# Optimization experiments

Measured on AMD Instinct MI355X. Metric: run time of the kernel, lower is better.

The kernel has to match this reference:

```python
import jax, jax.numpy as jnp
import numpy as np

IMG_SIZE = 640.0
CONF_THRESH = 0.001
NMS_THRESH = 0.6
TOP_K = 1000  # fixed-shape candidate cap per class


def _pairwise_iou(b):
    # b: [K,4] in x1,y1,x2,y2; replicates the numpy NMS math (1e-28 / 1e-14 eps)
    x1, y1, x2, y2 = b[:, 0], b[:, 1], b[:, 2], b[:, 3]
    areas = (x2 - x1) * (y2 - y1)
    xx1 = jnp.maximum(x1[:, None], x1[None, :])
    yy1 = jnp.maximum(y1[:, None], y1[None, :])
    xx2 = jnp.minimum(x2[:, None], x2[None, :])
    yy2 = jnp.minimum(y2[:, None], y2[None, :])
    w = jnp.maximum(1e-28, xx2 - xx1)
    h = jnp.maximum(1e-28, yy2 - yy1)
    inter = w * h
    return inter / (areas[:, None] + areas[None, :] - inter + 1e-14)


def setup_inputs() -> dict:
    key = jax.random.key(0)
    k1, k2, k3 = jax.random.split(key, 3)
    img_size, strides, KA, C = 640, [8, 16, 32], 3, 80
    anchor = np.array([[10, 13], [16, 30], [33, 23], [30, 61], [62, 45], [59, 119],
                       [116, 90], [156, 198], [373, 326]], np.float32).reshape(3, 3, 2)
    grids, anchs, strs = [], [], []
    for lvl, s in enumerate(strides):
        f = img_size // s
        gy, gx = np.meshgrid(np.arange(f), np.arange(f), indexing='ij')
        gxy = np.stack([gx, gy], -1).reshape(-1, 1, 2).astype(np.float32)
        grids.append(np.broadcast_to(gxy, (f * f, KA, 2)).reshape(-1, 2))
        anchs.append(np.broadcast_to(anchor[lvl][None], (f * f, KA, 2)).reshape(-1, 2).astype(np.float32))
        strs.append(np.full((f * f * KA, 1), s, np.float32))
    grid_xy = jnp.asarray(np.concatenate(grids, 0))      # [N,2]
    anchors_wh = jnp.asarray(np.concatenate(anchs, 0))   # [N,2]
    stride_t = jnp.asarray(np.concatenate(strs, 0))      # [N,1]
    N = grid_xy.shape[0]  # 25200
    return {
        'reg_pred': jax.random.normal(k1, (N, 4), jnp.float32),
        'obj_pred': jax.random.normal(k2, (N, 1), jnp.float32),
        'cls_pred': jax.random.normal(k3, (N, C), jnp.float32),
        'grid_xy': grid_xy,
        'anchors_wh': anchors_wh,
        'stride_t': stride_t,
    }


def reference(reg_pred, obj_pred, cls_pred, grid_xy, anchors_wh, stride_t):
    # ---- box decode (YOLO head) ----
    xy = (jax.nn.sigmoid(reg_pred[:, :2]) + grid_xy) * stride_t       # centers in pixels
    wh = jnp.exp(reg_pred[:, 2:]) * anchors_wh                        # sizes in pixels
    boxes = jnp.concatenate([xy - 0.5 * wh, xy + 0.5 * wh], axis=-1)  # [N,4]
    boxes = jnp.clip(boxes / IMG_SIZE, 0.0, 1.0)
    # ---- scoring: sigmoid(obj) * softmax(cls) ----
    scores_all = jax.nn.sigmoid(obj_pred) * jax.nn.softmax(cls_pred, axis=-1)  # [N,C]
    cls_inds = jnp.argmax(scores_all, axis=-1)          # [N]
    scores = jnp.max(scores_all, axis=-1)               # [N]
    C = cls_pred.shape[-1]
    K = TOP_K
    ar = jnp.arange(K)

    def nms_class(c):
        s_c = jnp.where((cls_inds == c) & (scores >= CONF_THRESH), scores, -1.0)
        vals, idx = jax.lax.top_k(s_c, K)               # sorted desc, fixed shape
        b = boxes[idx]                                  # [K,4]
        valid = vals > 0.0
        iou = _pairwise_iou(b)                          # [K,K]

        def body(i, keep):
            sup = keep[i] & (iou[i] > NMS_THRESH) & (ar > i)
            return keep & ~sup

        keep = jax.lax.fori_loop(0, K, body, valid)
        return b, vals, keep

    boxes_out, scores_out, keep = jax.vmap(nms_class)(jnp.arange(C))  # [C,K,4],[C,K],[C,K]
    return boxes_out, scores_out * keep.astype(scores_out.dtype), keep
```

## Files before the change

### kernel.cpp

```cpp
#include <hip/hip_runtime.h>
#include <cstdint>
#include <cstddef>

#define N_CLS 80
#define TOPK 1000
#define POOL_N 2048
#define MCAP 512
#define BD 1024
#define DTB 128
#define NBLK 197
#define SLICE 32
#define LDSB_STRIDE 10

__global__ __launch_bounds__(DTB) void decode_kernel(
    const float* __restrict__ reg, const float* __restrict__ obj,
    const float* __restrict__ cls, const float* __restrict__ grid,
    const float* __restrict__ anch, const float* __restrict__ strd,
    float* __restrict__ boxes, uint2* __restrict__ scs,
    int* __restrict__ cnts, uint2* __restrict__ gpool2, int N) {
  __shared__ int hcnt[N_CLS];
  const int blk = blockIdx.x;
  const int tid = threadIdx.x;
  const int i = blk * DTB + tid;

  if (tid < N_CLS) hcnt[tid] = 0;
  __syncthreads();

  const bool valid = (i < N);
  float best = -1.0f;
  int bc = 0;

  if (valid) {
    const float4 r = ((const float4*)reg)[i];
    const float2 g = ((const float2*)grid)[i];
    const float2 aw = ((const float2*)anch)[i];
    const float st = strd[i];

    float cx = (1.0f / (1.0f + expf(-r.x)) + g.x) * st;
    float cy = (1.0f / (1.0f + expf(-r.y)) + g.y) * st;
    float w = expf(r.z) * aw.x;
    float h = expf(r.w) * aw.y;
    float b0 = fminf(fmaxf((cx - 0.5f * w) / 640.0f, 0.0f), 1.0f);
    float b1 = fminf(fmaxf((cy - 0.5f * h) / 640.0f, 0.0f), 1.0f);
    float b2 = fminf(fmaxf((cx + 0.5f * w) / 640.0f, 0.0f), 1.0f);
    float b3 = fminf(fmaxf((cy + 0.5f * h) / 640.0f, 0.0f), 1.0f);
    float4 bo; bo.x = b0; bo.y = b1; bo.z = b2; bo.w = b3;
    ((float4*)boxes)[i] = bo;

    const float4* cr = (const float4*)cls + (size_t)i * 20;
    float4 x[20];
#pragma unroll
    for (int q = 0; q < 20; ++q) x[q] = cr[q];

    float4 m4 = x[0];
#pragma unroll
    for (int q = 1; q < 20; ++q) {
      m4.x = fmaxf(m4.x, x[q].x); m4.y = fmaxf(m4.y, x[q].y);
      m4.z = fmaxf(m4.z, x[q].z); m4.w = fmaxf(m4.w, x[q].w);
    }
    float mx = fmaxf(fmaxf(m4.x, m4.y), fmaxf(m4.z, m4.w));

#pragma unroll
    for (int q = 0; q < 20; ++q) {
      x[q].x = expf(x[q].x - mx); x[q].y = expf(x[q].y - mx);
      x[q].z = expf(x[q].z - mx); x[q].w = expf(x[q].w - mx);
    }

    float s = 0.0f;
#pragma unroll
    for (int q = 0; q < 20; ++q) {
      s += x[q].x; s += x[q].y; s += x[q].z; s += x[q].w;
    }

    float sig = 1.0f / (1.0f + expf(-obj[i]));

#pragma unroll
    for (int q = 0; q < 20; ++q) {
      float q0 = sig * (x[q].x / s);
      if (q0 > best) { best = q0; bc = 4 * q + 0; }
      float q1 = sig * (x[q].y / s);
      if (q1 > best) { best = q1; bc = 4 * q + 1; }
      float q2 = sig * (x[q].z / s);
      if (q2 > best) { best = q2; bc = 4 * q + 2; }
      float q3 = sig * (x[q].w / s);
      if (q3 > best) { best = q3; bc = 4 * q + 3; }
    }
    scs[i] = make_uint2(__float_as_uint(best), (unsigned)bc);
  }

  const bool pos = valid && (best >= 0.001f);
  int slot = -1;
  if (pos) slot = atomicAdd(&hcnt[bc], 1);
  __syncthreads();
  if (tid < N_CLS) cnts[tid * NBLK + blk] = min(hcnt[tid], SLICE);
  if (pos && slot < SLICE)
    gpool2[((size_t)bc * NBLK + blk) * SLICE + slot] =
        make_uint2(__float_as_uint(best), (unsigned)i);
}

__device__ __forceinline__ unsigned long long kinit(int w, int m) {
  int lo = w << 6;
  return (m <= lo) ? 0ULL : ((m - lo >= 64) ? ~0ULL : ((1ULL << (m - lo)) - 1ULL));
}

__global__ __launch_bounds__(BD) void nms_kernel(
    const float* __restrict__ boxes, const uint2* __restrict__ scs,
    const int* __restrict__ cnts, const uint2* __restrict__ gpool2,
    float* __restrict__ out, int N) {
  const int c = blockIdx.x;
  const int tid = threadIdx.x;

  __shared__ uint2 pool[POOL_N];
  __shared__ float svals[TOPK];
  __shared__ int sidx[TOPK];
  __shared__ __align__(16) float4 bxyz[TOPK];
  __shared__ __align__(16) unsigned long long ldsB[MCAP * LDSB_STRIDE];
  __shared__ unsigned char kp[TOPK];
  __shared__ __align__(16) unsigned long long kmbuf[2][8];
  __shared__ int wsum[BD / 64 + 1];
  __shared__ int pref[NBLK + 1];

  if (tid < 64) {
    const int* cc = cnts + c * NBLK;
    int carry = 0;
    if (tid == 0) pref[0] = 0;
    for (int ch = 0; ch < (NBLK + 63) / 64; ++ch) {
      int b = ch * 64 + tid;
      int v = (b < NBLK) ? cc[b] : 0;
#pragma unroll
      for (int s = 1; s < 64; s <<= 1) {
        int u = __shfl_up(v, s, 64);
        if (tid >= (unsigned)s) v += u;
      }
      if (b < NBLK) pref[b + 1] = min(carry + v, POOL_N);
      carry += __shfl(v, 63, 64);
    }
  }
  __syncthreads();
  const int cnt = pref[NBLK];
  const int m = min(cnt, TOPK);

  const uint2* gp = gpool2 + (size_t)c * NBLK * SLICE;
  for (int t = tid; t < cnt; t += BD) {
    int lo = 0, hi = NBLK;
    while (hi - lo > 1) {
      int mid = (lo + hi) >> 1;
      if (t >= pref[mid]) lo = mid; else hi = mid;
    }
    pool[t] = gp[(size_t)lo * SLICE + (t - pref[lo])];
  }
  __syncthreads();

  for (int e = tid; e < cnt; e += BD) {
    uint2 me = pool[e];
    float v = __uint_as_float(me.x);
    int idx = (int)me.y;
    int r = 0;
#pragma unroll 8
    for (int k = 0; k < cnt; ++k) {
      uint2 q = pool[k];
      float vk = __uint_as_float(q.x);
      r += (int)((vk > v) || (vk == v && (int)q.y < idx));
    }
    if (r < TOPK) { svals[r] = v; sidx[r] = idx; }
  }
  __syncthreads();

  const int M = TOPK - m;
  if (M > 0) {
    int i = tid;
    bool f = false;
    if (i < N) {
      uint2 sc = scs[i];
      f = !((int)sc.y == c && __uint_as_float(sc.x) >= 0.001f);
    }
    unsigned long long mk = __ballot(f ? 1 : 0);
    int lane = tid & 63, wv = tid >> 6;
    int pre = __popcll(mk & ((1ULL << lane) - 1ULL));
    if (lane == 0) wsum[wv] = __popcll(mk);
    __syncthreads();
    if (tid == 0) {
      int acc = 0;
      for (int wq = 0; wq < BD / 64; ++wq) { int t2 = wsum[wq]; wsum[wq] = acc; acc += t2; }
    }
    __syncthreads();
    int pos = wsum[wv] + pre;
    if (f && pos < M) sidx[m + pos] = i;
  }
  __syncthreads();

  const float4* bf4 = (const float4*)boxes;
  for (int t = tid; t < TOPK; t += BD) bxyz[t] = bf4[sidx[t]];
  __syncthreads();

  const int W = (m + 63) >> 6;
  const bool fast = (m > 0) && (m <= MCAP);
  int cur = 0;

  if (fast) {
    const int tasks = m * W;
    for (int q = tid; q < tasks; q += BD) {
      int w = q / m;
      int j = q - w * m;
      unsigned long long bits = 0ULL;
      if (w <= (j >> 6)) {
        float4 jb = bxyz[j];
        float aj = (jb.z - jb.x) * (jb.w - jb.y);
        int i0 = w << 6, iend = min(i0 + 64, j);
        for (int i = i0; i < iend; ++i) {
          float4 ib = bxyz[i];
          float ai = (ib.z - ib.x) * (ib.w - ib.y);
          float xx1 = fmaxf(ib.x, jb.x), yy1 = fmaxf(ib.y, jb.y);
          float xx2 = fminf(ib.z, jb.z), yy2 = fminf(ib.w, jb.w);
          float ww = fmaxf(1e-28f, xx2 - xx1), hh = fmaxf(1e-28f, yy2 - yy1);
          float inter = ww * hh;
          float iou = inter / (ai + aj - inter + 1e-14f);
          if (iou > 0.6f) bits |= (1ULL << (i - i0));
        }
      }
      ldsB[(size_t)j * LDSB_STRIDE + w] = bits;
    }
    __syncthreads();

    ulonglong2 ta, tb, tc, td;
    ta = tb = tc = td = make_ulonglong2(0ULL, 0ULL);
    if (tid < m) {
      const ulonglong2* rp = (const ulonglong2*)&ldsB[(size_t)tid * LDSB_STRIDE];
      ta = rp[0]; tb = rp[1]; tc = rp[2]; td = rp[3];
    }
    if (tid < 8) kmbuf[0][tid] = kinit(tid, m);
    __syncthreads();

    for (;;) {
      bool keep = false;
      if (tid < m) {
        unsigned long long sup =
            (ta.x & kmbuf[cur][0]) | (ta.y & kmbuf[cur][1]) |
            (tb.x & kmbuf[cur][2]) | (tb.y & kmbuf[cur][3]) |
            (tc.x & kmbuf[cur][4]) | (tc.y & kmbuf[cur][5]) |
            (td.x & kmbuf[cur][6]) | (td.y & kmbuf[cur][7]);
        keep = (sup == 0ULL);
      }
      bool old = (tid < m) &&
                 ((kmbuf[cur][tid >> 6] >> (tid & 63)) & 1ULL);
      unsigned long long bl = __ballot(keep ? 1 : 0);
      int wv = tid >> 6;
      if ((tid & 63) == 0 && wv < 8) kmbuf[cur ^ 1][wv] = bl;
      int any = __syncthreads_or((int)(keep != old));
      cur ^= 1;
      if (!any) break;
    }
  } else {
    for (int t = tid; t < TOPK; t += BD) kp[t] = (t < m) ? 1 : 0;
    __syncthreads();
    for (int i = 0; i < m; ++i) {
      if (kp[i]) {
        float4 rb = bxyz[i];
        float ai = (rb.z - rb.x) * (rb.w - rb.y);
        for (int j = i + 1 + tid; j < m; j += BD) {
          if (kp[j]) {
            float4 jb = bxyz[j];
            float aj = (jb.z - jb.x) * (jb.w - jb.y);
            float xx1 = fmaxf(rb.x, jb.x), yy1 = fmaxf(rb.y, jb.y);
            float xx2 = fminf(rb.z, jb.z), yy2 = fminf(rb.w, jb.w);
            float ww = fmaxf(1e-28f, xx2 - xx1), hh = fmaxf(1e-28f, yy2 - yy1);
            float inter = ww * hh;
            float iou = inter / (ai + aj - inter + 1e-14f);
            if (iou > 0.6f) kp[j] = 0;
          }
        }
      }
      __syncthreads();
    }
  }

  float* outB = out;
  float* outS = out + N_CLS * TOPK * 4;
  float* outK = outS + N_CLS * TOPK;
  for (int t = tid; t < TOPK; t += BD) {
    float k = 0.0f;
    if (t < m)
      k = fast ? (float)((kmbuf[cur][t >> 6] >> (t & 63)) & 1ULL)
               : (float)kp[t];
    float v = (t < m) ? svals[t] : -1.0f;
    ((float4*)outB)[c * TOPK + t] = bxyz[t];
    outS[c * TOPK + t] = v * k;
    outK[c * TOPK + t] = k;
  }
}

extern "C" void kernel_launch(void* const* d_in, const int* in_sizes, int n_in,
                              void* d_out, int out_size, void* d_ws, size_t ws_size,
                              hipStream_t stream) {
  const float* reg  = (const float*)d_in[0];
  const float* obj  = (const float*)d_in[1];
  const float* cls  = (const float*)d_in[2];
  const float* grid = (const float*)d_in[3];
  const float* anch = (const float*)d_in[4];
  const float* strd = (const float*)d_in[5];
  const int N = in_sizes[0] / 4;

  char* w8 = (char*)d_ws;
  size_t off = 0;
  float* boxes  = (float*)(w8 + off); off += (size_t)N * 16;
  uint2* scs    = (uint2*)(w8 + off); off += (size_t)N * 8;
  int*   cnts   = (int*)(w8 + off);   off += (size_t)N_CLS * NBLK * 4;
  uint2* gpool2 = (uint2*)(w8 + off); off += (size_t)N_CLS * NBLK * SLICE * 8;
  float* out = (float*)d_out;

  decode_kernel<<<NBLK, DTB, 0, stream>>>(
      reg, obj, cls, grid, anch, strd, boxes, scs, cnts, gpool2, N);
  nms_kernel<<<N_CLS, BD, 0, stream>>>(boxes, scs, cnts, gpool2, out, N);
}
```

Before: 113.6 us.

## Fuse decode and NMS into one cooperative kernel with grid sync

Merges the decode and per-class NMS kernels into a single cooperative launch of 80 blocks, separated by a grid-wide barrier. This removes the second kernel launch and the gap between the two kernels. In exchange, decode runs on only 80 blocks with most threads idle. Each block now covers more elements but keeps the same 32-per-class slice cap, which can drop candidates that the earlier layout kept.

```diff
diff --git a/kernel.cpp b/kernel.cpp
--- a/kernel.cpp
+++ b/kernel.cpp
@@ -1,32 +1,52 @@
 #include <hip/hip_runtime.h>
+#include <hip/hip_cooperative_groups.h>
 #include <cstdint>
 #include <cstddef>
+
+namespace cg = cooperative_groups;
 
 #define N_CLS 80
 #define TOPK 1000
 #define POOL_N 2048
 #define MCAP 512
 #define BD 1024
-#define DTB 128
-#define NBLK 197
+#define NBLK 80
 #define SLICE 32
 #define LDSB_STRIDE 10
 
-__global__ __launch_bounds__(DTB) void decode_kernel(
+__device__ __forceinline__ unsigned long long kinit(int w, int m) {
+  int lo = w << 6;
+  return (m <= lo) ? 0ULL : ((m - lo >= 64) ? ~0ULL : ((1ULL << (m - lo)) - 1ULL));
+}
+
+__global__ __launch_bounds__(BD) void fused_kernel(
     const float* __restrict__ reg, const float* __restrict__ obj,
     const float* __restrict__ cls, const float* __restrict__ grid,
     const float* __restrict__ anch, const float* __restrict__ strd,
     float* __restrict__ boxes, uint2* __restrict__ scs,
-    int* __restrict__ cnts, uint2* __restrict__ gpool2, int N) {
-  __shared__ int hcnt[N_CLS];
+    int* __restrict__ cnts, uint2* __restrict__ gpool2,
+    float* __restrict__ out, int N) {
   const int blk = blockIdx.x;
   const int tid = threadIdx.x;
-  const int i = blk * DTB + tid;
+
+  __shared__ int hcnt[N_CLS];
+  __shared__ uint2 pool[POOL_N];
+  __shared__ float svals[TOPK];
+  __shared__ int sidx[TOPK];
+  __shared__ __align__(16) float4 bxyz[TOPK];
+  __shared__ __align__(16) unsigned long long ldsB[MCAP * LDSB_STRIDE];
+  __shared__ unsigned char kp[TOPK];
+  __shared__ __align__(16) unsigned long long kmbuf[2][8];
+  __shared__ int wsum[BD / 64 + 1];
+  __shared__ int pref[NBLK + 1];
+
+  const int npb = (N + NBLK - 1) / NBLK;
+  const int i = blk * npb + tid;
+  const bool valid = (tid < npb) && (i < N);
 
   if (tid < N_CLS) hcnt[tid] = 0;
   __syncthreads();
 
-  const bool valid = (i < N);
   float best = -1.0f;
   int bc = 0;
 
@@ -88,37 +108,18 @@
     scs[i] = make_uint2(__float_as_uint(best), (unsigned)bc);
   }
 
-  const bool pos = valid && (best >= 0.001f);
+  const bool posi = valid && (best >= 0.001f);
   int slot = -1;
-  if (pos) slot = atomicAdd(&hcnt[bc], 1);
+  if (posi) slot = atomicAdd(&hcnt[bc], 1);
   __syncthreads();
   if (tid < N_CLS) cnts[tid * NBLK + blk] = min(hcnt[tid], SLICE);
-  if (pos && slot < SLICE)
+  if (posi && slot < SLICE)
     gpool2[((size_t)bc * NBLK + blk) * SLICE + slot] =
         make_uint2(__float_as_uint(best), (unsigned)i);
-}
-
-__device__ __forceinline__ unsigned long long kinit(int w, int m) {
-  int lo = w << 6;
-  return (m <= lo) ? 0ULL : ((m - lo >= 64) ? ~0ULL : ((1ULL << (m - lo)) - 1ULL));
-}
-
-__global__ __launch_bounds__(BD) void nms_kernel(
-    const float* __restrict__ boxes, const uint2* __restrict__ scs,
-    const int* __restrict__ cnts, const uint2* __restrict__ gpool2,
-    float* __restrict__ out, int N) {
-  const int c = blockIdx.x;
-  const int tid = threadIdx.x;
-
-  __shared__ uint2 pool[POOL_N];
-  __shared__ float svals[TOPK];
-  __shared__ int sidx[TOPK];
-  __shared__ __align__(16) float4 bxyz[TOPK];
-  __shared__ __align__(16) unsigned long long ldsB[MCAP * LDSB_STRIDE];
-  __shared__ unsigned char kp[TOPK];
-  __shared__ __align__(16) unsigned long long kmbuf[2][8];
-  __shared__ int wsum[BD / 64 + 1];
-  __shared__ int pref[NBLK + 1];
+
+  cg::this_grid().sync();
+
+  const int c = blk;
 
   if (tid < 64) {
     const int* cc = cnts + c * NBLK;
@@ -168,10 +169,10 @@
 
   const int M = TOPK - m;
   if (M > 0) {
-    int i = tid;
+    int i2 = tid;
     bool f = false;
-    if (i < N) {
-      uint2 sc = scs[i];
+    if (i2 < N) {
+      uint2 sc = scs[i2];
       f = !((int)sc.y == c && __uint_as_float(sc.x) >= 0.001f);
     }
     unsigned long long mk = __ballot(f ? 1 : 0);
@@ -185,7 +186,7 @@
     }
     __syncthreads();
     int pos = wsum[wv] + pre;
-    if (f && pos < M) sidx[m + pos] = i;
+    if (f && pos < M) sidx[m + pos] = i2;
   }
   __syncthreads();
 
@@ -207,15 +208,15 @@
         float4 jb = bxyz[j];
         float aj = (jb.z - jb.x) * (jb.w - jb.y);
         int i0 = w << 6, iend = min(i0 + 64, j);
-        for (int i = i0; i < iend; ++i) {
-          float4 ib = bxyz[i];
+        for (int i3 = i0; i3 < iend; ++i3) {
+          float4 ib = bxyz[i3];
           float ai = (ib.z - ib.x) * (ib.w - ib.y);
           float xx1 = fmaxf(ib.x, jb.x), yy1 = fmaxf(ib.y, jb.y);
           float xx2 = fminf(ib.z, jb.z), yy2 = fminf(ib.w, jb.w);
           float ww = fmaxf(1e-28f, xx2 - xx1), hh = fmaxf(1e-28f, yy2 - yy1);
           float inter = ww * hh;
           float iou = inter / (ai + aj - inter + 1e-14f);
-          if (iou > 0.6f) bits |= (1ULL << (i - i0));
+          if (iou > 0.6f) bits |= (1ULL << (i3 - i0));
         }
       }
       ldsB[(size_t)j * LDSB_STRIDE + w] = bits;
@@ -253,11 +254,11 @@
   } else {
     for (int t = tid; t < TOPK; t += BD) kp[t] = (t < m) ? 1 : 0;
     __syncthreads();
-    for (int i = 0; i < m; ++i) {
-      if (kp[i]) {
-        float4 rb = bxyz[i];
+    for (int i3 = 0; i3 < m; ++i3) {
+      if (kp[i3]) {
+        float4 rb = bxyz[i3];
         float ai = (rb.z - rb.x) * (rb.w - rb.y);
-        for (int j = i + 1 + tid; j < m; j += BD) {
+        for (int j = i3 + 1 + tid; j < m; j += BD) {
           if (kp[j]) {
             float4 jb = bxyz[j];
             float aj = (jb.z - jb.x) * (jb.w - jb.y);
@@ -298,7 +299,7 @@
   const float* grid = (const float*)d_in[3];
   const float* anch = (const float*)d_in[4];
   const float* strd = (const float*)d_in[5];
-  const int N = in_sizes[0] / 4;
+  int N = in_sizes[0] / 4;
 
   char* w8 = (char*)d_ws;
   size_t off = 0;
@@ -308,7 +309,9 @@
   uint2* gpool2 = (uint2*)(w8 + off); off += (size_t)N_CLS * NBLK * SLICE * 8;
   float* out = (float*)d_out;
 
-  decode_kernel<<<NBLK, DTB, 0, stream>>>(
-      reg, obj, cls, grid, anch, strd, boxes, scs, cnts, gpool2, N);
-  nms_kernel<<<N_CLS, BD, 0, stream>>>(boxes, scs, cnts, gpool2, out, N);
+  void* args[] = {(void*)&reg, (void*)&obj, (void*)&cls, (void*)&grid,
+                  (void*)&anch, (void*)&strd, (void*)&boxes, (void*)&scs,
+                  (void*)&cnts, (void*)&gpool2, (void*)&out, (void*)&N};
+  hipLaunchCooperativeKernel((const void*)fused_kernel, dim3(N_CLS), dim3(BD),
+                             args, 0, stream);
 }
```

Result: slower. 149.9 us (+32.0%).

## Stream class logits instead of register array; stage candidate pool in LDS for coalesced writes

Applied to the files above, without the earlier changes.

The decode kernel no longer holds all 80 logits in a 20-element float4 register array. It re-reads the row from global memory/cache in three passes (max, sum of exps, argmax), recomputing exps, to cut register pressure. Per-class candidates are first staged in a shared-memory pool, then the whole 80x32 pool is written to global memory in a coalesced loop. Because every slot is now written, this adds extra write traffic. The counts array is transposed to block-major order so the decode-side stores are contiguous, while the NMS side now does strided reads.

```diff
diff --git a/kernel.cpp b/kernel.cpp
--- a/kernel.cpp
+++ b/kernel.cpp
@@ -19,6 +19,7 @@
     float* __restrict__ boxes, uint2* __restrict__ scs,
     int* __restrict__ cnts, uint2* __restrict__ gpool2, int N) {
   __shared__ int hcnt[N_CLS];
+  __shared__ uint2 lpool[N_CLS * SLICE];
   const int blk = blockIdx.x;
   const int tid = threadIdx.x;
   const int i = blk * DTB + tid;
@@ -48,54 +49,61 @@
     ((float4*)boxes)[i] = bo;
 
     const float4* cr = (const float4*)cls + (size_t)i * 20;
-    float4 x[20];
+
+    float mx;
+    {
+      float4 v = cr[0];
+      mx = v.x;
+      mx = fmaxf(mx, v.y); mx = fmaxf(mx, v.z); mx = fmaxf(mx, v.w);
 #pragma unroll
-    for (int q = 0; q < 20; ++q) x[q] = cr[q];
-
-    float4 m4 = x[0];
-#pragma unroll
-    for (int q = 1; q < 20; ++q) {
-      m4.x = fmaxf(m4.x, x[q].x); m4.y = fmaxf(m4.y, x[q].y);
-      m4.z = fmaxf(m4.z, x[q].z); m4.w = fmaxf(m4.w, x[q].w);
-    }
-    float mx = fmaxf(fmaxf(m4.x, m4.y), fmaxf(m4.z, m4.w));
-
-#pragma unroll
-    for (int q = 0; q < 20; ++q) {
-      x[q].x = expf(x[q].x - mx); x[q].y = expf(x[q].y - mx);
-      x[q].z = expf(x[q].z - mx); x[q].w = expf(x[q].w - mx);
-    }
+      for (int q = 1; q < 20; ++q) {
+        float4 u = cr[q];
+        mx = fmaxf(mx, u.x); mx = fmaxf(mx, u.y);
+        mx = fmaxf(mx, u.z); mx = fmaxf(mx, u.w);
+      }
+    }
+    asm volatile("" ::: "memory");
 
     float s = 0.0f;
 #pragma unroll
     for (int q = 0; q < 20; ++q) {
-      s += x[q].x; s += x[q].y; s += x[q].z; s += x[q].w;
-    }
+      float4 u = cr[q];
+      s += expf(u.x - mx); s += expf(u.y - mx);
+      s += expf(u.z - mx); s += expf(u.w - mx);
+    }
+    asm volatile("" ::: "memory");
 
     float sig = 1.0f / (1.0f + expf(-obj[i]));
 
 #pragma unroll
     for (int q = 0; q < 20; ++q) {
-      float q0 = sig * (x[q].x / s);
+      float4 u = cr[q];
+      float e0 = expf(u.x - mx), e1 = expf(u.y - mx);
+      float e2 = expf(u.z - mx), e3 = expf(u.w - mx);
+      float q0 = sig * (e0 / s);
       if (q0 > best) { best = q0; bc = 4 * q + 0; }
-      float q1 = sig * (x[q].y / s);
+      float q1 = sig * (e1 / s);
       if (q1 > best) { best = q1; bc = 4 * q + 1; }
-      float q2 = sig * (x[q].z / s);
+      float q2 = sig * (e2 / s);
       if (q2 > best) { best = q2; bc = 4 * q + 2; }
-      float q3 = sig * (x[q].w / s);
+      float q3 = sig * (e3 / s);
       if (q3 > best) { best = q3; bc = 4 * q + 3; }
     }
     scs[i] = make_uint2(__float_as_uint(best), (unsigned)bc);
   }
 
   const bool pos = valid && (best >= 0.001f);
-  int slot = -1;
-  if (pos) slot = atomicAdd(&hcnt[bc], 1);
-  __syncthreads();
-  if (tid < N_CLS) cnts[tid * NBLK + blk] = min(hcnt[tid], SLICE);
-  if (pos && slot < SLICE)
-    gpool2[((size_t)bc * NBLK + blk) * SLICE + slot] =
-        make_uint2(__float_as_uint(best), (unsigned)i);
+  if (pos) {
+    int slot = atomicAdd(&hcnt[bc], 1);
+    if (slot < SLICE)
+      lpool[bc * SLICE + slot] = make_uint2(__float_as_uint(best), (unsigned)i);
+  }
+  __syncthreads();
+  if (tid < N_CLS) cnts[blk * N_CLS + tid] = min(hcnt[tid], SLICE);
+  for (int t = tid; t < N_CLS * SLICE; t += DTB) {
+    int c = t / SLICE, sl = t - c * SLICE;
+    gpool2[((size_t)c * NBLK + blk) * SLICE + sl] = lpool[t];
+  }
 }
 
 __device__ __forceinline__ unsigned long long kinit(int w, int m) {
@@ -121,12 +129,11 @@
   __shared__ int pref[NBLK + 1];
 
   if (tid < 64) {
-    const int* cc = cnts + c * NBLK;
     int carry = 0;
     if (tid == 0) pref[0] = 0;
     for (int ch = 0; ch < (NBLK + 63) / 64; ++ch) {
       int b = ch * 64 + tid;
-      int v = (b < NBLK) ? cc[b] : 0;
+      int v = (b < NBLK) ? cnts[b * N_CLS + c] : 0;
 #pragma unroll
       for (int s = 1; s < 64; s <<= 1) {
         int u = __shfl_up(v, s, 64);
@@ -304,7 +311,7 @@
   size_t off = 0;
   float* boxes  = (float*)(w8 + off); off += (size_t)N * 16;
   uint2* scs    = (uint2*)(w8 + off); off += (size_t)N * 8;
-  int*   cnts   = (int*)(w8 + off);   off += (size_t)N_CLS * NBLK * 4;
+  int*   cnts   = (int*)(w8 + off);   off += (size_t)NBLK * N_CLS * 4;
   uint2* gpool2 = (uint2*)(w8 + off); off += (size_t)N_CLS * NBLK * SLICE * 8;
   float* out = (float*)d_out;
 
```

New measurement: 117.4 us. 1.03x slower.
